# Kernel optimization log

Measured on AMD Instinct MI355X. Metric: run time of the kernel, lower is better.

Reference implementation:

```python
import jax, jax.numpy as jnp
import numpy as np
import math

IMAGE_SIZE = 256
VIEWING_ANGLE = 30.0  # degrees
NEAR = 0.1
FAR = 100.0
CHUNK = 50


def _look_at(vertices):
    # nr.look_at with at=origin, up=+y, eye from viewing_angle (as in __init__)
    eye = jnp.array([0.0, 0.0, -(1.0 / math.tan(math.radians(VIEWING_ANGLE)) + 1.0)],
                    dtype=vertices.dtype)
    at = jnp.zeros(3, dtype=vertices.dtype)
    up = jnp.array([0.0, 1.0, 0.0], dtype=vertices.dtype)
    z = at - eye
    z = z / jnp.linalg.norm(z)
    x = jnp.cross(up, z)
    x = x / jnp.linalg.norm(x)
    y = jnp.cross(z, x)
    y = y / jnp.linalg.norm(y)
    R = jnp.stack([x, y, z])  # [3,3] rows = camera axes
    return (vertices - eye) @ R.T


def _perspective(v):
    # nr.perspective: x,y divided by z*tan(angle); z (camera depth) kept
    width = math.tan(math.radians(VIEWING_ANGLE))
    z = v[..., 2]
    zs = jnp.where(jnp.abs(z) < 1e-5, 1e-5, z)  # avoid div-by-zero for behind-camera verts
    return jnp.stack([v[..., 0] / (zs * width), v[..., 1] / (zs * width), z], axis=-1)


def reference(vertices, faces):
    """Renderer.forward(vertices, faces, mode='depth'):
    fill_back -> look_at -> perspective -> vertices_to_faces -> rasterize_depth.
    Returns depth image [B, H, W] (FAR where no face covers the pixel)."""
    B = vertices.shape[0]
    # fill_back: append faces with reversed vertex order
    faces2 = jnp.concatenate([faces, faces[:, :, ::-1]], axis=1)  # [B, 2F, 3]
    v_scr = _perspective(_look_at(vertices))                      # [B, V, 3]
    # vertices_to_faces gather
    fv = jax.vmap(lambda v, f: v[f])(v_scr, faces2)               # [B, 2F, 3, 3]
    F2 = fv.shape[1]
    nsteps = F2 // CHUNK
    fv = fv.reshape(B, nsteps, CHUNK, 3, 3).transpose(1, 0, 2, 3, 4)  # [S,B,C,3,3]

    is_ = IMAGE_SIZE
    p = (2.0 * jnp.arange(is_, dtype=vertices.dtype) + 1.0 - is_) / is_  # pixel centers in (-1,1)
    py, px = jnp.meshgrid(p, p, indexing='ij')  # [H,W]

    def step(buf, f):  # f: [B,C,3,3]; z-buffer min over this face chunk
        x = f[..., 0][..., None, None]  # [B,C,3,1,1]
        y = f[..., 1][..., None, None]
        z = f[..., 2]                   # [B,C,3] camera-space depth per vertex
        x0, x1, x2 = x[:, :, 0], x[:, :, 1], x[:, :, 2]
        y0, y1, y2 = y[:, :, 0], y[:, :, 1], y[:, :, 2]
        area = (x1 - x0) * (y2 - y0) - (x2 - x0) * (y1 - y0)  # [B,C,1,1] signed 2*area
        area_s = jnp.where(jnp.abs(area) < 1e-8, 1e-8, area)
        # screen-space barycentric weights (edge functions / area)
        w0 = ((x1 - px) * (y2 - py) - (x2 - px) * (y1 - py)) / area_s
        w1 = ((x2 - px) * (y0 - py) - (x0 - px) * (y2 - py)) / area_s
        w2 = 1.0 - w0 - w1
        zc = jnp.maximum(z, 1e-4)  # safe for masked-out faces only
        # perspective-correct depth: z = 1 / (w0/z0 + w1/z1 + w2/z2)
        inv_z = (w0 / zc[:, :, 0, None, None] + w1 / zc[:, :, 1, None, None]
                 + w2 / zc[:, :, 2, None, None])
        zp = 1.0 / jnp.maximum(inv_z, 1e-6)
        front = jnp.all(z > NEAR, axis=-1)[..., None, None]
        inside = (w0 >= 0) & (w1 >= 0) & (w2 >= 0) & (jnp.abs(area) > 1e-8)
        valid = inside & front & (zp > NEAR) & (zp < FAR)
        zp = jnp.where(valid, zp, FAR)
        return jnp.minimum(buf, jnp.min(zp, axis=1)), None

    buf0 = jnp.full((B, is_, is_), FAR, dtype=vertices.dtype)
    depth, _ = jax.lax.scan(step, buf0, fv)
    return depth


def setup_inputs() -> dict:
    key = jax.random.key(0)
    kv, kf = jax.random.split(key)
    B, NV, NF = 1, 2502, 5000
    # mesh roughly within the camera frustum (eye at z~-2.73 looking at origin)
    vertices = 0.35 * jax.random.normal(kv, (B, NV, 3), dtype=jnp.float32)
    faces = jax.random.randint(kf, (B, NF, 3), 0, NV, dtype=jnp.int32)
    return {"vertices": vertices, "faces": faces}
```

## Files before the change

### kernel.cpp

```cpp
#include <hip/hip_runtime.h>

#define IS 256
#define NEARV 0.1f
#define FARV 100.0f
#define NTX 16
#define NTILES 256
#define CAP 5120
#define CHK 32
#define CPT ((CAP + CHK - 1) / CHK)
#define RBLOCKS 2048
#define RWAVES (RBLOCKS * 4)
#define MAXITEMS (NTILES * CPT)

__global__ void kinit(unsigned int* __restrict__ zb, int* __restrict__ count,
                      int* __restrict__ misc) {
    int i = blockIdx.x * 256 + threadIdx.x;
    zb[i] = 0x42C80000u;
    if (i < NTILES) count[i] = 0;
    if (i == NTILES) misc[0] = 0;
}

__launch_bounds__(256)
__global__ void kbinprep(const float* __restrict__ verts, const int* __restrict__ faces,
                         float4* __restrict__ fd, int* __restrict__ count,
                         unsigned short* __restrict__ list, int* __restrict__ misc,
                         int* __restrict__ items, int nf) {
    __shared__ int scnt[NTILES];
    __shared__ int sbase[NTILES];
    __shared__ int slast;
    const int tid = threadIdx.x;
    for (int t = tid; t < NTILES; t += 256) scnt[t] = 0;
    __syncthreads();

    const int f = blockIdx.x * 256 + tid;
    int kx0 = 0, kx1 = -1, ky0 = 0, ky1 = -1;
    float bxmin = 0.f, bymin = 0.f, bxmax = -1.f, bymax = -1.f;
    if (f < nf) {
        int i0 = faces[f * 3 + 0];
        int i1 = faces[f * 3 + 1];
        int i2 = faces[f * 3 + 2];
        float z0 = verts[i0 * 3 + 2] + 2.7320508075688772f;
        float z1 = verts[i1 * 3 + 2] + 2.7320508075688772f;
        float z2 = verts[i2 * 3 + 2] + 2.7320508075688772f;
        bool front = (z0 > NEARV) && (z1 > NEARV) && (z2 > NEARV);
        float zs0 = (fabsf(z0) < 1e-5f) ? 1e-5f : z0;
        float zs1 = (fabsf(z1) < 1e-5f) ? 1e-5f : z1;
        float zs2 = (fabsf(z2) < 1e-5f) ? 1e-5f : z2;
        float d0 = zs0 * 0.57735026918962576f;
        float d1 = zs1 * 0.57735026918962576f;
        float d2 = zs2 * 0.57735026918962576f;
        float x0 = verts[i0 * 3 + 0] / d0;
        float y0 = verts[i0 * 3 + 1] / d0;
        float x1 = verts[i1 * 3 + 0] / d1;
        float y1 = verts[i1 * 3 + 1] / d1;
        float x2 = verts[i2 * 3 + 0] / d2;
        float y2 = verts[i2 * 3 + 1] / d2;
        float area = (x1 - x0) * (y2 - y0) - (x2 - x0) * (y1 - y0);
        if (front && (fabsf(area) > 1e-8f)) {
            bxmin = fminf(x0, fminf(x1, x2));
            bxmax = fmaxf(x0, fmaxf(x1, x2));
            bymin = fminf(y0, fminf(y1, y2));
            bymax = fmaxf(y0, fmaxf(y1, y2));
            float ia = 1.0f / area;
            float iz0 = 1.0f / fmaxf(z0, 1e-4f);
            float iz1 = 1.0f / fmaxf(z1, 1e-4f);
            float iz2 = 1.0f / fmaxf(z2, 1e-4f);
            float4* o = fd + (size_t)f * 4;
            o[0] = make_float4(x0, y0, x1, y1);
            o[1] = make_float4(x2, y2, ia, iz0);
            o[2] = make_float4(iz1, iz2, 0.0f, 0.0f);
            float tminx = fminf(fmaxf((bxmin * 256.0f + 225.0f) * (1.0f / 32.0f), -2.0f), 17.0f);
            float tmaxx = fminf(fmaxf((bxmax * 256.0f + 255.0f) * (1.0f / 32.0f), -2.0f), 17.0f);
            float tminy = fminf(fmaxf((bymin * 256.0f + 225.0f) * (1.0f / 32.0f), -2.0f), 17.0f);
            float tmaxy = fminf(fmaxf((bymax * 256.0f + 255.0f) * (1.0f / 32.0f), -2.0f), 17.0f);
            kx0 = max(0, (int)ceilf(tminx) - 1);
            kx1 = min(NTX - 1, (int)floorf(tmaxx) + 1);
            ky0 = max(0, (int)ceilf(tminy) - 1);
            ky1 = min(NTX - 1, (int)floorf(tmaxy) + 1);
        }
    }
    for (int ky = ky0; ky <= ky1; ++ky) {
        float py_lo = (float)(32 * ky - 255) * (1.0f / 256.0f);
        float py_hi = (float)(32 * ky - 225) * (1.0f / 256.0f);
        if (!(bymin <= py_hi && bymax >= py_lo)) continue;
        for (int kx = kx0; kx <= kx1; ++kx) {
            float px_lo = (float)(32 * kx - 255) * (1.0f / 256.0f);
            float px_hi = (float)(32 * kx - 225) * (1.0f / 256.0f);
            if (bxmin <= px_hi && bxmax >= px_lo) atomicAdd(&scnt[ky * NTX + kx], 1);
        }
    }
    __syncthreads();
    for (int t = tid; t < NTILES; t += 256) {
        int c = scnt[t];
        sbase[t] = (c > 0) ? atomicAdd(&count[t], c) : 0;
        scnt[t] = 0;
    }
    __syncthreads();
    for (int ky = ky0; ky <= ky1; ++ky) {
        float py_lo = (float)(32 * ky - 255) * (1.0f / 256.0f);
        float py_hi = (float)(32 * ky - 225) * (1.0f / 256.0f);
        if (!(bymin <= py_hi && bymax >= py_lo)) continue;
        for (int kx = kx0; kx <= kx1; ++kx) {
            float px_lo = (float)(32 * kx - 255) * (1.0f / 256.0f);
            float px_hi = (float)(32 * kx - 225) * (1.0f / 256.0f);
            if (bxmin <= px_hi && bxmax >= px_lo) {
                int t = ky * NTX + kx;
                int slot = sbase[t] + atomicAdd(&scnt[t], 1);
                list[(size_t)t * CAP + slot] = (unsigned short)f;
            }
        }
    }
    __syncthreads();
    __threadfence();
    if (tid == 0) slast = (atomicAdd(&misc[0], 1) == (int)gridDim.x - 1) ? 1 : 0;
    __syncthreads();
    if (!slast) return;
    __threadfence();
    int c = __hip_atomic_load(&count[tid], __ATOMIC_RELAXED, __HIP_MEMORY_SCOPE_AGENT);
    int nch = (c + CHK - 1) / CHK;
    scnt[tid] = nch;
    __syncthreads();
    for (int d = 1; d < NTILES; d <<= 1) {
        int v = (tid >= d) ? scnt[tid - d] : 0;
        __syncthreads();
        scnt[tid] += v;
        __syncthreads();
    }
    int off = scnt[tid] - nch;
    if (tid == NTILES - 1) misc[64] = scnt[tid];
    for (int k = 0; k < nch; ++k) {
        int n = min(CHK, c - k * CHK);
        items[off + k] = (tid << 16) | (n << 8) | k;
    }
}

__launch_bounds__(256)
__global__ void kraster(const float4* __restrict__ fd, const unsigned short* __restrict__ list,
                        const int* __restrict__ items, const int* __restrict__ misc,
                        unsigned int* __restrict__ zb) {
    __shared__ float4 sdata[4][CHK * 3];
    const int wslot = __builtin_amdgcn_readfirstlane(threadIdx.x >> 6);
    const int wid = blockIdx.x * 4 + wslot;
    const int lane = threadIdx.x & 63;
    const int cx = lane & 15;
    const int ry = lane >> 4;
    const int ni = __builtin_amdgcn_readfirstlane(misc[64]);
    float4* sd = &sdata[wslot][0];

    for (int it = wid; it < ni; it += RWAVES) {
        const int pk = __builtin_amdgcn_readfirstlane(items[it]);
        const int tile = pk >> 16;
        const int n = (pk >> 8) & 0xff;
        const int chunk = pk & 0xff;
        const int bx = tile & 15;
        const int by = tile >> 4;
        const int j = bx * 16 + cx;
        const float px = ((float)(2 * j + 1) - 256.0f) * (1.0f / 256.0f);
        float py[4];
        int row[4];
        unsigned int zcur[4];
#pragma unroll
        for (int r = 0; r < 4; ++r) {
            row[r] = by * 16 + ry + 4 * r;
            py[r] = ((float)(2 * row[r] + 1) - 256.0f) * (1.0f / 256.0f);
            zcur[r] = zb[row[r] * IS + j];
        }
        const unsigned short* lp = list + (size_t)tile * CAP + chunk * CHK;
        if (lane < n) {
            const int fidx = lp[lane];
            const float4* p = fd + (size_t)fidx * 4;
            float4 b0 = p[0];
            float4 b1 = p[1];
            float4 b2 = p[2];
            sd[lane * 3 + 0] = b0;
            sd[lane * 3 + 1] = b1;
            sd[lane * 3 + 2] = b2;
        }
        asm volatile("s_waitcnt lgkmcnt(0)" ::: "memory");

        float mx[4] = {0.0f, 0.0f, 0.0f, 0.0f};

#pragma unroll 2
        for (int e = 0; e < n; ++e) {
            float4 a0 = sd[e * 3 + 0];
            float4 a1 = sd[e * 3 + 1];
            float4 a2 = sd[e * 3 + 2];
            float dx0 = a0.x - px, dx1 = a0.z - px, dx2 = a1.x - px;
#pragma unroll
            for (int r = 0; r < 4; ++r) {
                float dy0 = a0.y - py[r], dy1 = a0.w - py[r], dy2 = a1.y - py[r];
                float e0 = dx1 * dy2 - dx2 * dy1;
                float e1 = dx2 * dy0 - dx0 * dy2;
                float w0 = e0 * a1.z;
                float w1 = e1 * a1.z;
                float w2 = 1.0f - w0 - w1;
                float invz = w0 * a1.w + w1 * a2.x + w2 * a2.y;
                float invzc = fmaxf(invz, 1e-6f);
                float wmin = fminf(fminf(w0, w1), w2);
                bool ok = (wmin >= 0.0f) && (invzc < 10.0f) && (invzc > 0.01f);
                if (ok) mx[r] = fmaxf(mx[r], invzc);
            }
        }
#pragma unroll
        for (int r = 0; r < 4; ++r) {
            if (mx[r] > 0.0f) {
                float zp = 1.0f / mx[r];
                unsigned int zbits = __float_as_uint(zp);
                if (zbits < zcur[r]) atomicMin(&zb[row[r] * IS + j], zbits);
            }
        }
    }
}

extern "C" void kernel_launch(void* const* d_in, const int* in_sizes, int n_in,
                              void* d_out, int out_size, void* d_ws, size_t ws_size,
                              hipStream_t stream) {
    const float* verts = (const float*)d_in[0];
    const int* faces = (const int*)d_in[1];
    unsigned int* zb = (unsigned int*)d_out;

    const int nf = in_sizes[1] / 3;

    char* ws = (char*)d_ws;
    size_t off = 0;
    float4* fd = (float4*)(ws + off);            off += (size_t)nf * 64;
    off = (off + 255) & ~(size_t)255;
    int* count = (int*)(ws + off);               off += NTILES * 4;
    off = (off + 255) & ~(size_t)255;
    int* misc = (int*)(ws + off);                off += 512;
    int* items = (int*)(ws + off);               off += (size_t)MAXITEMS * 4;
    off = (off + 255) & ~(size_t)255;
    unsigned short* list = (unsigned short*)(ws + off);

    const int nb = (nf + 255) / 256;

    kinit<<<(IS * IS) / 256, 256, 0, stream>>>(zb, count, misc);
    kbinprep<<<nb, 256, 0, stream>>>(verts, faces, fd, count, list, misc, items, nf);
    kraster<<<RBLOCKS, 256, 0, stream>>>(fd, list, items, misc, zb);
}
```

Before: 107.8 us.

## Fuse z-buffer init into binning and bin per-tile threads over shared bboxes

Removes the separate init kernel: the z-buffer fill moves into the binning kernel and the counters are cleared with a memset. Binning is restructured so each thread owns one tile and scans the block's 256 face bounding boxes from shared memory, replacing per-face loops with shared-memory atomics. This drops the two-pass shared atomic scheme and issues at most one global atomic per tile per block. In exchange every thread does 512 bbox tests, and list order within a tile becomes deterministic.

Result: slower. 136.2 us (+26.4%).

```diff
diff --git a/kernel.cpp b/kernel.cpp
--- a/kernel.cpp
+++ b/kernel.cpp
@@ -12,29 +12,26 @@
 #define RWAVES (RBLOCKS * 4)
 #define MAXITEMS (NTILES * CPT)
 
-__global__ void kinit(unsigned int* __restrict__ zb, int* __restrict__ count,
-                      int* __restrict__ misc) {
-    int i = blockIdx.x * 256 + threadIdx.x;
-    zb[i] = 0x42C80000u;
-    if (i < NTILES) count[i] = 0;
-    if (i == NTILES) misc[0] = 0;
-}
-
 __launch_bounds__(256)
 __global__ void kbinprep(const float* __restrict__ verts, const int* __restrict__ faces,
                          float4* __restrict__ fd, int* __restrict__ count,
                          unsigned short* __restrict__ list, int* __restrict__ misc,
-                         int* __restrict__ items, int nf) {
+                         int* __restrict__ items, unsigned int* __restrict__ zb, int nf) {
+    __shared__ float4 sbb[256];
     __shared__ int scnt[NTILES];
-    __shared__ int sbase[NTILES];
     __shared__ int slast;
     const int tid = threadIdx.x;
-    for (int t = tid; t < NTILES; t += 256) scnt[t] = 0;
-    __syncthreads();
-
-    const int f = blockIdx.x * 256 + tid;
-    int kx0 = 0, kx1 = -1, ky0 = 0, ky1 = -1;
-    float bxmin = 0.f, bymin = 0.f, bxmax = -1.f, bymax = -1.f;
+    const int bid = blockIdx.x;
+    const int nb = gridDim.x;
+
+    {
+        uint4* zb4 = (uint4*)zb;
+        const uint4 farv = make_uint4(0x42C80000u, 0x42C80000u, 0x42C80000u, 0x42C80000u);
+        for (int i = bid * 256 + tid; i < (IS * IS) / 4; i += nb * 256) zb4[i] = farv;
+    }
+
+    const int f = bid * 256 + tid;
+    float4 mybb = make_float4(3.0e8f, 3.0e8f, -3.0e8f, -3.0e8f);
     if (f < nf) {
         int i0 = faces[f * 3 + 0];
         int i1 = faces[f * 3 + 1];
@@ -57,10 +54,10 @@
         float y2 = verts[i2 * 3 + 1] / d2;
         float area = (x1 - x0) * (y2 - y0) - (x2 - x0) * (y1 - y0);
         if (front && (fabsf(area) > 1e-8f)) {
-            bxmin = fminf(x0, fminf(x1, x2));
-            bxmax = fmaxf(x0, fmaxf(x1, x2));
-            bymin = fminf(y0, fminf(y1, y2));
-            bymax = fmaxf(y0, fmaxf(y1, y2));
+            float bxmin = fminf(x0, fminf(x1, x2));
+            float bxmax = fmaxf(x0, fmaxf(x1, x2));
+            float bymin = fminf(y0, fminf(y1, y2));
+            float bymax = fmaxf(y0, fmaxf(y1, y2));
             float ia = 1.0f / area;
             float iz0 = 1.0f / fmaxf(z0, 1e-4f);
             float iz1 = 1.0f / fmaxf(z1, 1e-4f);
@@ -69,50 +66,40 @@
             o[0] = make_float4(x0, y0, x1, y1);
             o[1] = make_float4(x2, y2, ia, iz0);
             o[2] = make_float4(iz1, iz2, 0.0f, 0.0f);
-            float tminx = fminf(fmaxf((bxmin * 256.0f + 225.0f) * (1.0f / 32.0f), -2.0f), 17.0f);
-            float tmaxx = fminf(fmaxf((bxmax * 256.0f + 255.0f) * (1.0f / 32.0f), -2.0f), 17.0f);
-            float tminy = fminf(fmaxf((bymin * 256.0f + 225.0f) * (1.0f / 32.0f), -2.0f), 17.0f);
-            float tmaxy = fminf(fmaxf((bymax * 256.0f + 255.0f) * (1.0f / 32.0f), -2.0f), 17.0f);
-            kx0 = max(0, (int)ceilf(tminx) - 1);
-            kx1 = min(NTX - 1, (int)floorf(tmaxx) + 1);
-            ky0 = max(0, (int)ceilf(tminy) - 1);
-            ky1 = min(NTX - 1, (int)floorf(tmaxy) + 1);
-        }
-    }
-    for (int ky = ky0; ky <= ky1; ++ky) {
-        float py_lo = (float)(32 * ky - 255) * (1.0f / 256.0f);
-        float py_hi = (float)(32 * ky - 225) * (1.0f / 256.0f);
-        if (!(bymin <= py_hi && bymax >= py_lo)) continue;
-        for (int kx = kx0; kx <= kx1; ++kx) {
-            float px_lo = (float)(32 * kx - 255) * (1.0f / 256.0f);
-            float px_hi = (float)(32 * kx - 225) * (1.0f / 256.0f);
-            if (bxmin <= px_hi && bxmax >= px_lo) atomicAdd(&scnt[ky * NTX + kx], 1);
-        }
-    }
-    __syncthreads();
-    for (int t = tid; t < NTILES; t += 256) {
-        int c = scnt[t];
-        sbase[t] = (c > 0) ? atomicAdd(&count[t], c) : 0;
-        scnt[t] = 0;
-    }
-    __syncthreads();
-    for (int ky = ky0; ky <= ky1; ++ky) {
-        float py_lo = (float)(32 * ky - 255) * (1.0f / 256.0f);
-        float py_hi = (float)(32 * ky - 225) * (1.0f / 256.0f);
-        if (!(bymin <= py_hi && bymax >= py_lo)) continue;
-        for (int kx = kx0; kx <= kx1; ++kx) {
-            float px_lo = (float)(32 * kx - 255) * (1.0f / 256.0f);
-            float px_hi = (float)(32 * kx - 225) * (1.0f / 256.0f);
-            if (bxmin <= px_hi && bxmax >= px_lo) {
-                int t = ky * NTX + kx;
-                int slot = sbase[t] + atomicAdd(&scnt[t], 1);
-                list[(size_t)t * CAP + slot] = (unsigned short)f;
-            }
-        }
-    }
+            mybb = make_float4(bxmin, bymin, bxmax, bymax);
+        }
+    }
+    sbb[tid] = mybb;
+    __syncthreads();
+
+    const int tkx = tid & 15;
+    const int tky = tid >> 4;
+    const float px_lo = (float)(32 * tkx - 255) * (1.0f / 256.0f);
+    const float px_hi = (float)(32 * tkx - 225) * (1.0f / 256.0f);
+    const float py_lo = (float)(32 * tky - 255) * (1.0f / 256.0f);
+    const float py_hi = (float)(32 * tky - 225) * (1.0f / 256.0f);
+
+    int cnt = 0;
+#pragma unroll 4
+    for (int i = 0; i < 256; ++i) {
+        float4 bb = sbb[i];
+        if (bb.y <= py_hi && bb.w >= py_lo && bb.x <= px_hi && bb.z >= px_lo) ++cnt;
+    }
+    const int sbase = (cnt > 0) ? atomicAdd(&count[tid], cnt) : 0;
+    const int fbase = bid * 256;
+    int k = 0;
+#pragma unroll 4
+    for (int i = 0; i < 256; ++i) {
+        float4 bb = sbb[i];
+        if (bb.y <= py_hi && bb.w >= py_lo && bb.x <= px_hi && bb.z >= px_lo) {
+            list[(size_t)tid * CAP + sbase + k] = (unsigned short)(fbase + i);
+            ++k;
+        }
+    }
+
     __syncthreads();
     __threadfence();
-    if (tid == 0) slast = (atomicAdd(&misc[0], 1) == (int)gridDim.x - 1) ? 1 : 0;
+    if (tid == 0) slast = (atomicAdd(&misc[0], 1) == nb - 1) ? 1 : 0;
     __syncthreads();
     if (!slast) return;
     __threadfence();
@@ -128,9 +115,9 @@
     }
     int off = scnt[tid] - nch;
     if (tid == NTILES - 1) misc[64] = scnt[tid];
-    for (int k = 0; k < nch; ++k) {
-        int n = min(CHK, c - k * CHK);
-        items[off + k] = (tid << 16) | (n << 8) | k;
+    for (int q = 0; q < nch; ++q) {
+        int n = min(CHK, c - q * CHK);
+        items[off + q] = (tid << 16) | (n << 8) | q;
     }
 }
 
@@ -226,7 +213,6 @@
     float4* fd = (float4*)(ws + off);            off += (size_t)nf * 64;
     off = (off + 255) & ~(size_t)255;
     int* count = (int*)(ws + off);               off += NTILES * 4;
-    off = (off + 255) & ~(size_t)255;
     int* misc = (int*)(ws + off);                off += 512;
     int* items = (int*)(ws + off);               off += (size_t)MAXITEMS * 4;
     off = (off + 255) & ~(size_t)255;
@@ -234,7 +220,7 @@
 
     const int nb = (nf + 255) / 256;
 
-    kinit<<<(IS * IS) / 256, 256, 0, stream>>>(zb, count, misc);
-    kbinprep<<<nb, 256, 0, stream>>>(verts, faces, fd, count, list, misc, items, nf);
+    hipMemsetAsync(count, 0, NTILES * 4 + 512, stream);
+    kbinprep<<<nb, 256, 0, stream>>>(verts, faces, fd, count, list, misc, items, zb, nf);
     kraster<<<RBLOCKS, 256, 0, stream>>>(fd, list, items, misc, zb);
 }
```
